# Optimization experiments

Hardware: AMD Instinct MI355X
Metric: run time of the kernel (lower is better)

Reference implementation:

```python
import jax, jax.numpy as jnp
import numpy as np

N_NODES = 50000
N_EDGES = 1_600_000
IN_DIM = 64
HID_DIM = 64
OUT_DIM = 64


def setup_inputs() -> dict:
    key = jax.random.key(0)
    k = jax.random.split(key, 7)
    feat = jax.random.normal(k[0], (N_NODES, IN_DIM), dtype=jnp.float32)
    src = jax.random.randint(k[1], (N_EDGES,), 0, N_NODES, dtype=jnp.int32)
    dst = jax.random.randint(k[2], (N_EDGES,), 0, N_NODES, dtype=jnp.int32)
    # nn.init.normal_(weight, std=0.1); bias default uniform ~ small, use 0.1*randn
    W1 = 0.1 * jax.random.normal(k[3], (HID_DIM, IN_DIM), dtype=jnp.float32)
    b1 = 0.1 * jax.random.normal(k[4], (HID_DIM,), dtype=jnp.float32)
    W2 = 0.1 * jax.random.normal(k[5], (OUT_DIM, HID_DIM), dtype=jnp.float32)
    b2 = 0.1 * jax.random.normal(k[6], (OUT_DIM,), dtype=jnp.float32)
    return {"feat": feat, "src": src, "dst": dst, "W1": W1, "b1": b1, "W2": W2, "b2": b2}


def _gnn_layer(h, src, dst, W, b):
    # copy_u + sum: gather source-node features along edges, scatter-sum to dst
    agg = jax.ops.segment_sum(h[src], dst, num_segments=N_NODES)  # [N, d_in]
    return agg @ W.T + b  # nn.Linear


def reference(feat, src, dst, W1, b1, W2, b2):
    h = _gnn_layer(feat, src, dst, W1, b1)
    h = jnp.tanh(h)
    h = _gnn_layer(h, src, dst, W2, b2)
    return h
```

## Files before the change

### kernel.cpp

```cpp
#include <hip/hip_runtime.h>

#define N_NODES 50000
#define N_EDGES 1600000
#define DIM 64
#define NBK 196
#define BIN_BLOCKS 391
#define CSR_CAP 12288
#define QCAP 3072
#define GEMM_BLOCKS 197
#define NB_AGG8 6250

__device__ __forceinline__ unsigned short f2bf(float f) {
    union { float f; unsigned u; } v; v.f = f;
    unsigned r = v.u + 0x7FFF + ((v.u >> 16) & 1);
    return (unsigned short)(r >> 16);
}
__device__ __forceinline__ float bf2f(unsigned short h) {
    union { unsigned u; float f; } v; v.u = ((unsigned)h) << 16;  return v.f;
}
__device__ __forceinline__ float blo(unsigned u) {
    union { unsigned u; float f; } v; v.u = u << 16; return v.f;
}
__device__ __forceinline__ float bhi(unsigned u) {
    union { unsigned u; float f; } v; v.u = u & 0xFFFF0000u; return v.f;
}

__global__ __launch_bounds__(256) void bin_and_gemm1(const int* __restrict__ src,
                                                     const int* __restrict__ dst,
                                                     int* __restrict__ bcur,
                                                     int* __restrict__ binned,
                                                     const float* __restrict__ X,
                                                     const float* __restrict__ W,
                                                     unsigned short* __restrict__ T) {
    __shared__ int cnt[NBK];
    __shared__ int lofs[NBK];
    __shared__ int shiftv[NBK];
    __shared__ int sb[256];
    __shared__ int stag[4096];
    __shared__ unsigned char stb[4096];
    __shared__ float Ws[64 * 64];
    int tid = threadIdx.x;

    if (blockIdx.x >= BIN_BLOCKS) {
#pragma unroll
        for (int j = 0; j < 16; ++j) Ws[j * 256 + tid] = W[j * 256 + tid];
        __syncthreads();

        int n = (blockIdx.x - BIN_BLOCKS) * 256 + tid;
        if (n > N_NODES) return;
        ushort4* tp = (ushort4*)(T + (size_t)n * 64);
        if (n == N_NODES) {
            ushort4 z = {0, 0, 0, 0};
#pragma unroll
            for (int k = 0; k < 16; ++k) tp[k] = z;
            return;
        }

        float4 x[16];
        const float4* xp = (const float4*)(X + (size_t)n * 64);
#pragma unroll
        for (int k = 0; k < 16; ++k) x[k] = xp[k];

        for (int fg = 0; fg < 16; ++fg) {
            float r[4];
#pragma unroll
            for (int fi = 0; fi < 4; ++fi) {
                int f = fg * 4 + fi;
                float acc = 0.f;
#pragma unroll
                for (int k4 = 0; k4 < 16; ++k4) {
                    float4 w = *(const float4*)&Ws[f * 64 + k4 * 4];
                    float4 xv = x[k4];
                    acc += xv.x * w.x + xv.y * w.y + xv.z * w.z + xv.w * w.w;
                }
                r[fi] = acc;
            }
            ushort4 o;
            o.x = f2bf(r[0]); o.y = f2bf(r[1]); o.z = f2bf(r[2]); o.w = f2bf(r[3]);
            tp[fg] = o;
        }
        return;
    }

    if (tid < NBK) cnt[tid] = 0;
    __syncthreads();

    int base = blockIdx.x * 4096;
    int nedge = N_EDGES - base;
    if (nedge > 4096) nedge = 4096;

    int myb[16], myr[16], myp[16];
#pragma unroll
    for (int i = 0; i < 16; ++i) {
        int e = base + i * 256 + tid;
        myb[i] = -1;
        if (e < N_EDGES) {
            int s = src[e], d = dst[e];
            int b = d >> 8;
            myb[i] = b;
            myp[i] = ((d & 255) << 16) | s;
            myr[i] = atomicAdd(&cnt[b], 1);
        }
    }
    __syncthreads();

    int c = (tid < NBK) ? cnt[tid] : 0;
    sb[tid] = c;
    __syncthreads();
    for (int off = 1; off < 256; off <<= 1) {
        int u = (tid >= off) ? sb[tid - off] : 0;
        __syncthreads();
        sb[tid] += u;
        __syncthreads();
    }
    if (tid < NBK) {
        lofs[tid] = sb[tid] - c;
        if (c) shiftv[tid] = tid * CSR_CAP + atomicAdd(&bcur[tid * 16], c) - lofs[tid];
    }
    __syncthreads();

#pragma unroll
    for (int i = 0; i < 16; ++i) {
        if (myb[i] >= 0) {
            int idx = lofs[myb[i]] + myr[i];
            stag[idx] = myp[i];
            stb[idx] = (unsigned char)myb[i];
        }
    }
    __syncthreads();

    for (int i = tid; i < nedge; i += 256)
        binned[i + shiftv[stb[i]]] = stag[i];
}

__global__ __launch_bounds__(256) void build_csr(const int* __restrict__ binned,
                                                 const int* __restrict__ bcur,
                                                 unsigned* __restrict__ nodeinfo,
                                                 unsigned short* __restrict__ csr16) {
    __shared__ int cnt[64], cnt2[64], ofs[64], sb[64];
    __shared__ int qtot;
    int tid = threadIdx.x;
    int b = blockIdx.x >> 2;
    int q = blockIdx.x & 3;
    int ibase = b * CSR_CAP;
    int qbase = (b * 4 + q) * QCAP;
    int m = bcur[b * 16];
    if (m > CSR_CAP) m = CSR_CAP;
    if (tid < 64) { cnt[tid] = 0; cnt2[tid] = 0; }
    __syncthreads();

    for (int i = tid; i < m; i += 256) {
        int dl = (binned[ibase + i] >> 16) & 255;
        if ((dl >> 6) == q) atomicAdd(&cnt[dl & 63], 1);
    }
    __syncthreads();

    int v = 0;
    if (tid < 64) { v = (cnt[tid] + 15) & ~15; sb[tid] = v; }
    __syncthreads();
    for (int off = 1; off < 64; off <<= 1) {
        int u = (tid >= off && tid < 64) ? sb[tid - off] : 0;
        __syncthreads();
        if (tid < 64) sb[tid] += u;
        __syncthreads();
    }
    if (tid < 64) {
        ofs[tid] = sb[tid] - v;
        int node = (b << 8) + (q << 6) + tid;
        if (node < N_NODES)
            nodeinfo[node] = ((unsigned)v << 23) | (unsigned)(qbase + ofs[tid]);
    }
    if (tid == 63) qtot = sb[63];
    __syncthreads();

    int qt = qtot;
    for (int i = tid; i < qt; i += 256) csr16[qbase + i] = (unsigned short)N_NODES;
    __syncthreads();

    for (int i = tid; i < m; i += 256) {
        int p = binned[ibase + i];
        int dl = (p >> 16) & 255;
        if ((dl >> 6) == q) {
            int r = atomicAdd(&cnt2[dl & 63], 1);
            csr16[qbase + ofs[dl & 63] + r] = (unsigned short)(p & 0xFFFF);
        }
    }
}

#define ACC8(d)                                                     \
    a0 += blo(d.x); a1 += bhi(d.x); a2 += blo(d.y); a3 += bhi(d.y); \
    a4 += blo(d.z); a5 += bhi(d.z); a6 += blo(d.w); a7 += bhi(d.w);

__global__ __launch_bounds__(512) void agg_fuse1(const unsigned short* __restrict__ T,
                                                 const unsigned short* __restrict__ csr,
                                                 const unsigned* __restrict__ nodeinfo,
                                                 const float* __restrict__ b1,
                                                 const float* __restrict__ W2,
                                                 unsigned short* __restrict__ T2) {
    __shared__ __align__(16) float4 W2t4[1024];
    __shared__ __align__(16) float part[8][8][72];
    int tid = threadIdx.x;
    int w = tid >> 6;
    int lane = tid & 63;
    int g8 = lane >> 3;
    int fs = lane & 7;
    int node = blockIdx.x * 8 + w;

    for (int L4 = tid; L4 < 1024; L4 += 512) {
        int k4 = L4 >> 6, f = L4 & 63;
        W2t4[L4] = *(const float4*)(W2 + f * 64 + k4 * 4);
    }

    unsigned info = __builtin_nontemporal_load(nodeinfo + node);
    float bias = b1[lane];
    int pos = (int)(info & 0x7FFFFFu);
    int nch = (int)(info >> 23) >> 3;
    const unsigned short* ip = csr + pos + g8;
    const uint4* Tp = (const uint4*)T;
    float a0 = 0.f, a1 = 0.f, a2 = 0.f, a3 = 0.f, a4 = 0.f, a5 = 0.f, a6 = 0.f, a7 = 0.f;
    int c = 0;
    for (; c + 4 <= nch; c += 4) {
        int j0 = __builtin_nontemporal_load(ip + c * 8);
        int j1 = __builtin_nontemporal_load(ip + c * 8 + 8);
        int j2 = __builtin_nontemporal_load(ip + c * 8 + 16);
        int j3 = __builtin_nontemporal_load(ip + c * 8 + 24);
        uint4 d0 = Tp[j0 * 8 + fs];
        uint4 d1 = Tp[j1 * 8 + fs];
        uint4 d2 = Tp[j2 * 8 + fs];
        uint4 d3 = Tp[j3 * 8 + fs];
        ACC8(d0) ACC8(d1) ACC8(d2) ACC8(d3)
    }
    if (c < nch) {
        int j0 = __builtin_nontemporal_load(ip + c * 8);
        int j1 = __builtin_nontemporal_load(ip + c * 8 + 8);
        uint4 d0 = Tp[j0 * 8 + fs];
        uint4 d1 = Tp[j1 * 8 + fs];
        ACC8(d0) ACC8(d1)
    }
    float4 pa = {a0, a1, a2, a3};
    float4 pb = {a4, a5, a6, a7};
    *(float4*)&part[w][g8][fs * 8] = pa;
    *(float4*)&part[w][g8][fs * 8 + 4] = pb;
    __syncthreads();

    float acc = bias;
#pragma unroll
    for (int g = 0; g < 8; ++g) acc += part[w][g][lane];

    float e = __expf(2.f * acc);
    part[w][0][lane] = 1.f - 2.f / (e + 1.f);

    const float* hrow = &part[w][0][0];
    float tf = 0.f;
#pragma unroll
    for (int k4 = 0; k4 < 16; ++k4) {
        float4 hv = *(const float4*)(hrow + k4 * 4);
        float4 wv = W2t4[k4 * 64 + lane];
        tf += hv.x * wv.x + hv.y * wv.y + hv.z * wv.z + hv.w * wv.w;
    }
    T2[(size_t)node * DIM + lane] = f2bf(tf);

    if (blockIdx.x == 0 && tid < 64)
        T2[(size_t)N_NODES * DIM + tid] = 0;
}

__global__ __launch_bounds__(512) void agg_out(const unsigned short* __restrict__ T,
                                               const unsigned short* __restrict__ csr,
                                               const unsigned* __restrict__ nodeinfo,
                                               const float* __restrict__ bias,
                                               float* __restrict__ outp) {
    __shared__ __align__(16) float part[8][8][72];
    int tid = threadIdx.x;
    int w = tid >> 6;
    int lane = tid & 63;
    int g8 = lane >> 3;
    int fs = lane & 7;
    int node = blockIdx.x * 8 + w;

    unsigned info = __builtin_nontemporal_load(nodeinfo + node);
    float bv = bias[lane];
    int pos = (int)(info & 0x7FFFFFu);
    int nch = (int)(info >> 23) >> 3;
    const unsigned short* ip = csr + pos + g8;
    const uint4* Tp = (const uint4*)T;
    float a0 = 0.f, a1 = 0.f, a2 = 0.f, a3 = 0.f, a4 = 0.f, a5 = 0.f, a6 = 0.f, a7 = 0.f;
    int c = 0;
    for (; c + 4 <= nch; c += 4) {
        int j0 = __builtin_nontemporal_load(ip + c * 8);
        int j1 = __builtin_nontemporal_load(ip + c * 8 + 8);
        int j2 = __builtin_nontemporal_load(ip + c * 8 + 16);
        int j3 = __builtin_nontemporal_load(ip + c * 8 + 24);
        uint4 d0 = Tp[j0 * 8 + fs];
        uint4 d1 = Tp[j1 * 8 + fs];
        uint4 d2 = Tp[j2 * 8 + fs];
        uint4 d3 = Tp[j3 * 8 + fs];
        ACC8(d0) ACC8(d1) ACC8(d2) ACC8(d3)
    }
    if (c < nch) {
        int j0 = __builtin_nontemporal_load(ip + c * 8);
        int j1 = __builtin_nontemporal_load(ip + c * 8 + 8);
        uint4 d0 = Tp[j0 * 8 + fs];
        uint4 d1 = Tp[j1 * 8 + fs];
        ACC8(d0) ACC8(d1)
    }
    float4 pa = {a0, a1, a2, a3};
    float4 pb = {a4, a5, a6, a7};
    *(float4*)&part[w][g8][fs * 8] = pa;
    *(float4*)&part[w][g8][fs * 8 + 4] = pb;

    float acc = bv;
#pragma unroll
    for (int g = 0; g < 8; ++g) acc += part[w][g][lane];
    __builtin_nontemporal_store(acc, outp + (size_t)node * DIM + lane);
}

extern "C" void kernel_launch(void* const* d_in, const int* in_sizes, int n_in,
                              void* d_out, int out_size, void* d_ws, size_t ws_size,
                              hipStream_t stream) {
    const float* feat = (const float*)d_in[0];
    const int*   src  = (const int*)d_in[1];
    const int*   dst  = (const int*)d_in[2];
    const float* W1   = (const float*)d_in[3];
    const float* b1   = (const float*)d_in[4];
    const float* W2   = (const float*)d_in[5];
    const float* b2   = (const float*)d_in[6];
    float* out = (float*)d_out;

    int*            binned   = (int*)d_ws;
    unsigned short* csr16    = (unsigned short*)(binned + NBK * CSR_CAP);
    unsigned*       nodeinfo = (unsigned*)(csr16 + NBK * 4 * QCAP);
    int*            bcur     = (int*)(nodeinfo + N_NODES);
    unsigned short* t        = (unsigned short*)(bcur + NBK * 16 + 8);
    unsigned short* t2       = t + (size_t)(N_NODES + 1) * 64;

    hipMemsetAsync(bcur, 0, NBK * 16 * sizeof(int), stream);
    bin_and_gemm1<<<BIN_BLOCKS + GEMM_BLOCKS, 256, 0, stream>>>(
        src, dst, bcur, binned, feat, W1, t);
    build_csr<<<NBK * 4, 256, 0, stream>>>(binned, bcur, nodeinfo, csr16);

    agg_fuse1<<<NB_AGG8, 512, 0, stream>>>(t, csr16, nodeinfo, b1, W2, t2);

    agg_out<<<NB_AGG8, 512, 0, stream>>>(t2, csr16, nodeinfo, b2, out);
}
```

Baseline: 224.6 us.

## Split aggregation by feature quarters and move tanh+GEMM2 into separate kernel

The aggregation kernels now split each node's 64 features into four 16-wide quarters, each handled by its own block, with 16 edge groups per node instead of 8. Consecutive blocks cover different quarters of the same nodes, which is meant to shrink the per-pass gather working set and improve cache locality. Tanh and the second linear layer move out of the first aggregation into a standalone per-node kernel that reads an fp32 intermediate buffer. This costs an extra launch and an extra fp32 write and read of the hidden activations. The new GEMM kernel holds a 64-float row per thread, which adds register pressure.

```diff
diff --git a/kernel.cpp b/kernel.cpp
--- a/kernel.cpp
+++ b/kernel.cpp
@@ -8,7 +8,8 @@
 #define CSR_CAP 12288
 #define QCAP 3072
 #define GEMM_BLOCKS 197
-#define NB_AGG8 6250
+#define NB_AGGQ 12500
+#define TG_BLOCKS 196
 
 __device__ __forceinline__ unsigned short f2bf(float f) {
     union { float f; unsigned u; } v; v.f = f;
@@ -191,127 +192,109 @@
     a0 += blo(d.x); a1 += bhi(d.x); a2 += blo(d.y); a3 += bhi(d.y); \
     a4 += blo(d.z); a5 += bhi(d.z); a6 += blo(d.w); a7 += bhi(d.w);
 
-__global__ __launch_bounds__(512) void agg_fuse1(const unsigned short* __restrict__ T,
-                                                 const unsigned short* __restrict__ csr,
-                                                 const unsigned* __restrict__ nodeinfo,
-                                                 const float* __restrict__ b1,
-                                                 const float* __restrict__ W2,
-                                                 unsigned short* __restrict__ T2) {
-    __shared__ __align__(16) float4 W2t4[1024];
-    __shared__ __align__(16) float part[8][8][72];
+template <bool ADD_BIAS_ONLY>
+__global__ __launch_bounds__(512) void agg_q(const unsigned short* __restrict__ T,
+                                             const unsigned short* __restrict__ csr,
+                                             const unsigned* __restrict__ nodeinfo,
+                                             const float* __restrict__ bias,
+                                             float* __restrict__ dstp) {
+    __shared__ float part[8][2][16][17];
     int tid = threadIdx.x;
-    int w = tid >> 6;
-    int lane = tid & 63;
-    int g8 = lane >> 3;
-    int fs = lane & 7;
-    int node = blockIdx.x * 8 + w;
-
-    for (int L4 = tid; L4 < 1024; L4 += 512) {
-        int k4 = L4 >> 6, f = L4 & 63;
-        W2t4[L4] = *(const float4*)(W2 + f * 64 + k4 * 4);
-    }
+    int w = tid >> 6, lane = tid & 63;
+    int ns = lane >> 5;
+    int g  = (lane >> 1) & 15;
+    int fs = lane & 1;
+    int q  = blockIdx.x & 3;
+    int c  = ((blockIdx.x >> 3) << 1) | ((blockIdx.x >> 2) & 1);
+    int node = c * 16 + w * 2 + ns;
 
     unsigned info = __builtin_nontemporal_load(nodeinfo + node);
-    float bias = b1[lane];
     int pos = (int)(info & 0x7FFFFFu);
-    int nch = (int)(info >> 23) >> 3;
-    const unsigned short* ip = csr + pos + g8;
+    int nt16 = (int)(info >> 23) >> 4;
+    const unsigned short* ip = csr + pos + g;
     const uint4* Tp = (const uint4*)T;
+    int qo = q * 2 + fs;
     float a0 = 0.f, a1 = 0.f, a2 = 0.f, a3 = 0.f, a4 = 0.f, a5 = 0.f, a6 = 0.f, a7 = 0.f;
-    int c = 0;
-    for (; c + 4 <= nch; c += 4) {
-        int j0 = __builtin_nontemporal_load(ip + c * 8);
-        int j1 = __builtin_nontemporal_load(ip + c * 8 + 8);
-        int j2 = __builtin_nontemporal_load(ip + c * 8 + 16);
-        int j3 = __builtin_nontemporal_load(ip + c * 8 + 24);
-        uint4 d0 = Tp[j0 * 8 + fs];
-        uint4 d1 = Tp[j1 * 8 + fs];
-        uint4 d2 = Tp[j2 * 8 + fs];
-        uint4 d3 = Tp[j3 * 8 + fs];
-        ACC8(d0) ACC8(d1) ACC8(d2) ACC8(d3)
-    }
-    if (c < nch) {
-        int j0 = __builtin_nontemporal_load(ip + c * 8);
-        int j1 = __builtin_nontemporal_load(ip + c * 8 + 8);
-        uint4 d0 = Tp[j0 * 8 + fs];
-        uint4 d1 = Tp[j1 * 8 + fs];
+    int k = 0;
+    for (; k + 2 <= nt16; k += 2) {
+        int j0 = __builtin_nontemporal_load(ip + k * 16);
+        int j1 = __builtin_nontemporal_load(ip + k * 16 + 16);
+        uint4 d0 = Tp[(size_t)j0 * 8 + qo];
+        uint4 d1 = Tp[(size_t)j1 * 8 + qo];
         ACC8(d0) ACC8(d1)
     }
-    float4 pa = {a0, a1, a2, a3};
-    float4 pb = {a4, a5, a6, a7};
-    *(float4*)&part[w][g8][fs * 8] = pa;
-    *(float4*)&part[w][g8][fs * 8 + 4] = pb;
-    __syncthreads();
-
-    float acc = bias;
-#pragma unroll
-    for (int g = 0; g < 8; ++g) acc += part[w][g][lane];
-
-    float e = __expf(2.f * acc);
-    part[w][0][lane] = 1.f - 2.f / (e + 1.f);
-
-    const float* hrow = &part[w][0][0];
-    float tf = 0.f;
-#pragma unroll
-    for (int k4 = 0; k4 < 16; ++k4) {
-        float4 hv = *(const float4*)(hrow + k4 * 4);
-        float4 wv = W2t4[k4 * 64 + lane];
-        tf += hv.x * wv.x + hv.y * wv.y + hv.z * wv.z + hv.w * wv.w;
-    }
-    T2[(size_t)node * DIM + lane] = f2bf(tf);
-
-    if (blockIdx.x == 0 && tid < 64)
-        T2[(size_t)N_NODES * DIM + tid] = 0;
-}
-
-__global__ __launch_bounds__(512) void agg_out(const unsigned short* __restrict__ T,
-                                               const unsigned short* __restrict__ csr,
-                                               const unsigned* __restrict__ nodeinfo,
-                                               const float* __restrict__ bias,
-                                               float* __restrict__ outp) {
-    __shared__ __align__(16) float part[8][8][72];
+    if (k < nt16) {
+        int j0 = __builtin_nontemporal_load(ip + k * 16);
+        uint4 d0 = Tp[(size_t)j0 * 8 + qo];
+        ACC8(d0)
+    }
+    float* pp = &part[w][ns][g][fs * 8];
+    pp[0] = a0; pp[1] = a1; pp[2] = a2; pp[3] = a3;
+    pp[4] = a4; pp[5] = a5; pp[6] = a6; pp[7] = a7;
+
+    if (lane < 32) {
+        int f = lane & 15, n2 = lane >> 4;
+        float s = bias[q * 16 + f];
+#pragma unroll
+        for (int gg = 0; gg < 16; ++gg) s += part[w][n2][gg][f];
+        __builtin_nontemporal_store(
+            s, dstp + (size_t)(c * 16 + w * 2 + n2) * 64 + q * 16 + f);
+    }
+    (void)ADD_BIAS_ONLY;
+}
+
+__global__ __launch_bounds__(256) void tanh_gemm2(const float* __restrict__ aggf,
+                                                  const float* __restrict__ W2,
+                                                  unsigned short* __restrict__ T2) {
+    __shared__ float Ws[64 * 64];
     int tid = threadIdx.x;
-    int w = tid >> 6;
-    int lane = tid & 63;
-    int g8 = lane >> 3;
-    int fs = lane & 7;
-    int node = blockIdx.x * 8 + w;
-
-    unsigned info = __builtin_nontemporal_load(nodeinfo + node);
-    float bv = bias[lane];
-    int pos = (int)(info & 0x7FFFFFu);
-    int nch = (int)(info >> 23) >> 3;
-    const unsigned short* ip = csr + pos + g8;
-    const uint4* Tp = (const uint4*)T;
-    float a0 = 0.f, a1 = 0.f, a2 = 0.f, a3 = 0.f, a4 = 0.f, a5 = 0.f, a6 = 0.f, a7 = 0.f;
-    int c = 0;
-    for (; c + 4 <= nch; c += 4) {
-        int j0 = __builtin_nontemporal_load(ip + c * 8);
-        int j1 = __builtin_nontemporal_load(ip + c * 8 + 8);
-        int j2 = __builtin_nontemporal_load(ip + c * 8 + 16);
-        int j3 = __builtin_nontemporal_load(ip + c * 8 + 24);
-        uint4 d0 = Tp[j0 * 8 + fs];
-        uint4 d1 = Tp[j1 * 8 + fs];
-        uint4 d2 = Tp[j2 * 8 + fs];
-        uint4 d3 = Tp[j3 * 8 + fs];
-        ACC8(d0) ACC8(d1) ACC8(d2) ACC8(d3)
-    }
-    if (c < nch) {
-        int j0 = __builtin_nontemporal_load(ip + c * 8);
-        int j1 = __builtin_nontemporal_load(ip + c * 8 + 8);
-        uint4 d0 = Tp[j0 * 8 + fs];
-        uint4 d1 = Tp[j1 * 8 + fs];
-        ACC8(d0) ACC8(d1)
-    }
-    float4 pa = {a0, a1, a2, a3};
-    float4 pb = {a4, a5, a6, a7};
-    *(float4*)&part[w][g8][fs * 8] = pa;
-    *(float4*)&part[w][g8][fs * 8 + 4] = pb;
-
-    float acc = bv;
-#pragma unroll
-    for (int g = 0; g < 8; ++g) acc += part[w][g][lane];
-    __builtin_nontemporal_store(acc, outp + (size_t)node * DIM + lane);
+#pragma unroll
+    for (int j = 0; j < 16; ++j) Ws[j * 256 + tid] = W2[j * 256 + tid];
+    __syncthreads();
+
+    int n = blockIdx.x * 256 + tid;
+    if (n > N_NODES) return;
+    uint2* tp = (uint2*)(T2 + (size_t)n * 64);
+    if (n == N_NODES) {
+        uint2 z = {0, 0};
+#pragma unroll
+        for (int k = 0; k < 16; ++k) tp[k] = z;
+        return;
+    }
+
+    float4 h[16];
+    const float4* xp = (const float4*)(aggf + (size_t)n * 64);
+#pragma unroll
+    for (int k = 0; k < 16; ++k) {
+        float4 v = xp[k];
+        float4 t;
+        float e;
+        e = __expf(2.f * v.x); t.x = 1.f - 2.f / (e + 1.f);
+        e = __expf(2.f * v.y); t.y = 1.f - 2.f / (e + 1.f);
+        e = __expf(2.f * v.z); t.z = 1.f - 2.f / (e + 1.f);
+        e = __expf(2.f * v.w); t.w = 1.f - 2.f / (e + 1.f);
+        h[k] = t;
+    }
+
+    for (int fg = 0; fg < 16; ++fg) {
+        float r[4];
+#pragma unroll
+        for (int fi = 0; fi < 4; ++fi) {
+            int f = fg * 4 + fi;
+            float acc = 0.f;
+#pragma unroll
+            for (int k4 = 0; k4 < 16; ++k4) {
+                float4 wv = *(const float4*)&Ws[f * 64 + k4 * 4];
+                float4 hv = h[k4];
+                acc += hv.x * wv.x + hv.y * wv.y + hv.z * wv.z + hv.w * wv.w;
+            }
+            r[fi] = acc;
+        }
+        unsigned lo = ((unsigned)f2bf(r[1]) << 16) | (unsigned)f2bf(r[0]);
+        unsigned hi = ((unsigned)f2bf(r[3]) << 16) | (unsigned)f2bf(r[2]);
+        uint2 o; o.x = lo; o.y = hi;
+        *(tp + fg) = o;
+    }
 }
 
 extern "C" void kernel_launch(void* const* d_in, const int* in_sizes, int n_in,
@@ -332,13 +315,16 @@
     int*            bcur     = (int*)(nodeinfo + N_NODES);
     unsigned short* t        = (unsigned short*)(bcur + NBK * 16 + 8);
     unsigned short* t2       = t + (size_t)(N_NODES + 1) * 64;
-
-    hipMemsetAsync(bcur, 0, NBK * 16 * sizeof(int), stream);
+    float*          aggf     = (float*)(t2 + (size_t)(N_NODES + 1) * 64);
+
+    (void)hipMemsetAsync(bcur, 0, NBK * 16 * sizeof(int), stream);
     bin_and_gemm1<<<BIN_BLOCKS + GEMM_BLOCKS, 256, 0, stream>>>(
         src, dst, bcur, binned, feat, W1, t);
     build_csr<<<NBK * 4, 256, 0, stream>>>(binned, bcur, nodeinfo, csr16);
 
-    agg_fuse1<<<NB_AGG8, 512, 0, stream>>>(t, csr16, nodeinfo, b1, W2, t2);
-
-    agg_out<<<NB_AGG8, 512, 0, stream>>>(t2, csr16, nodeinfo, b2, out);
-}
+    agg_q<false><<<NB_AGGQ, 512, 0, stream>>>(t, csr16, nodeinfo, b1, aggf);
+
+    tanh_gemm2<<<TG_BLOCKS, 256, 0, stream>>>(aggf, W2, t2);
+
+    agg_q<true><<<NB_AGGQ, 512, 0, stream>>>(t2, csr16, nodeinfo, b2, out);
+}
```

Result: slower. 307.6 us (+36.9%).
